# Performance work log

Hardware: AMD Instinct MI355X
Metric: run time of the kernel (lower is better)

Reference implementation:

```python
import jax, jax.numpy as jnp
import numpy as np

A = 200000   # atoms
B = 400000   # directed bonds
H = 300      # hidden_size
AF = 133     # atom_fdim
BF = 147     # bond_fdim
DEPTH = 4    # message passing depth -> DEPTH-1 W_h layers
M = 4096     # molecules in batch


def setup_inputs() -> dict:
    key = jax.random.key(0)
    ks = jax.random.split(key, 10)
    s = 0.05
    f_atoms = jax.random.normal(ks[0], (A, AF), jnp.float32)
    f_bonds = jax.random.normal(ks[1], (B, BF), jnp.float32)
    b_src = jax.random.randint(ks[2], (B,), 0, A, jnp.int32)
    b_dst = jax.random.randint(ks[3], (B,), 0, A, jnp.int32)
    # reverse-bond pairing: bond 2i <-> 2i+1
    b2revb = (jnp.arange(B, dtype=jnp.int32) ^ 1)
    mol_ids = jnp.sort(jax.random.randint(ks[4], (A,), 0, M, jnp.int32))
    W_i_atom = jax.random.normal(ks[5], (AF, H), jnp.float32) * s
    W_i_bond = jax.random.normal(ks[6], (BF, H), jnp.float32) * s
    W_h = jax.random.normal(ks[7], (DEPTH - 1, H, H), jnp.float32) * s
    W_o = jax.random.normal(ks[8], (3 * H, H), jnp.float32) * s
    b_o = jnp.zeros((H,), jnp.float32)
    return dict(f_atoms=f_atoms, f_bonds=f_bonds, W_i_atom=W_i_atom,
                W_i_bond=W_i_bond, W_h=W_h, W_o=W_o, b_o=b_o,
                b_src=b_src, b_dst=b_dst, b2revb=b2revb, mol_ids=mol_ids)


def reference(f_atoms, f_bonds, W_i_atom, W_i_bond, W_h, W_o, b_o,
              b_src, b_dst, b2revb, mol_ids):
    relu = jax.nn.relu
    input_atom = relu(f_atoms @ W_i_atom)   # [A, H]
    input_bond = relu(f_bonds @ W_i_bond)   # [B, H]

    def step(message, Wd):
        # scatter-sum incoming bond messages onto destination atoms
        a_msg = jax.ops.segment_sum(message, b_dst, num_segments=A)  # [A, H]
        # gather back to bonds, subtract reverse-bond message (D-MPNN)
        m = a_msg[b_src] - message[b2revb]                           # [B, H]
        return relu(input_bond + m @ Wd), None

    message, _ = jax.lax.scan(step, input_bond, W_h)  # DEPTH-1 iterations

    a_msg = jax.ops.segment_sum(message, b_dst, num_segments=A)      # [A, H]
    a_input = jnp.concatenate([input_atom, a_msg, input_atom * a_msg], axis=-1)
    atom_h = relu(a_input @ W_o + b_o)                               # [A, H]

    # mean readout per molecule
    sums = jax.ops.segment_sum(atom_h, mol_ids, num_segments=M)      # [M, H]
    counts = jax.ops.segment_sum(jnp.ones((A,), atom_h.dtype), mol_ids, num_segments=M)
    return sums / jnp.clip(counts, 1.0)[:, None]
```

## Files before the change

### kernel.cpp

```cpp
#include <hip/hip_runtime.h>
#include <stdint.h>

#define H   300
#define HP  320
#define CAP 32

using bf8 = __attribute__((ext_vector_type(8))) short;
using s4  = __attribute__((ext_vector_type(4))) short;
using f4  = __attribute__((ext_vector_type(4))) float;

__device__ __forceinline__ float bf2f(unsigned short u){
    union { unsigned int i; float f; } v; v.i = ((unsigned int)u) << 16; return v.f;
}
__device__ __forceinline__ unsigned short f2bf(float x){
    unsigned int u = __builtin_bit_cast(unsigned int, x);
    u = (u + 0x7FFFu + ((u >> 16) & 1u)) >> 16;
    return (unsigned short)u;
}

__global__ void fill_k(const int* __restrict__ b_dst, int* __restrict__ cnt,
                       int* __restrict__ bucket, int nB){
    int e = blockIdx.x * 256 + threadIdx.x;
    if (e >= nB) return;
    int d = b_dst[e];
    int slot = atomicAdd(&cnt[d], 1);
    if (slot < CAP) bucket[(long)d * CAP + slot] = e;
}

__global__ void prep_wt(const float* __restrict__ W, unsigned short* __restrict__ Wt,
                        int Kact, int Kp){
    int idx = blockIdx.x * 256 + threadIdx.x;
    if (idx >= 320 * Kp) return;
    int t  = idx / (320 * 32);
    int r  = idx % (320 * 32);
    int n  = r / 32, kk = r % 32;
    int k  = t * 32 + kk;
    float v = (n < H && k < Kact) ? W[(long)k * H + n] : 0.f;
    Wt[idx] = f2bf(v);
}

__global__ void prep_wto(const float* __restrict__ W, unsigned short* __restrict__ Wt){
    int idx = blockIdx.x * 256 + threadIdx.x;
    if (idx >= 320 * 960) return;
    int t  = idx / (320 * 32);
    int r  = idx % (320 * 32);
    int n  = r / 32, kk = r % 32;
    int k  = t * 32 + kk;
    int sec = k / HP, ksec = k % HP;
    float v = (n < H && ksec < H) ? W[((long)sec * H + ksec) * H + n] : 0.f;
    Wt[idx] = f2bf(v);
}

__global__ __launch_bounds__(256)
void conv_in(const float* __restrict__ X, int rows, int Kact,
             unsigned short* __restrict__ Y){
    int t = blockIdx.x * 256 + threadIdx.x;
    if (t >= rows * 20) return;
    int row = t / 20, c = t % 20;
    int k0 = c * 8;
    bf8 v;
    #pragma unroll
    for (int j = 0; j < 8; j++){
        int k = k0 + j;
        float f = (k < Kact) ? X[(long)row * Kact + k] : 0.f;
        v[j] = (short)f2bf(f);
    }
    *(bf8*)(Y + (long)row * 160 + k0) = v;
}

template<int RL, int SEC, int EPI>
__global__ __launch_bounds__(256, 4)
void gemm_k(const unsigned short* __restrict__ A0,
            const unsigned short* __restrict__ A1,
            const unsigned short* __restrict__ A2,
            const unsigned short* __restrict__ Wt,
            const float* __restrict__ b_o,
            unsigned short* __restrict__ outb,
            int nTiles)
{
    constexpr int KS     = RL / 32;
    constexpr int TS     = SEC * KS;
    constexpr int CHUNKS = RL / 8;
    constexpr int XM     = (RL == 320) ? 7 : 3;
    constexpr int NCH    = 32 * CHUNKS;
    constexpr int ROWB   = RL * 2;

    __shared__ char lds[32 * ROWB];

    const int tid  = threadIdx.x;
    const int w    = tid >> 6;
    const int lane = tid & 63;
    const int lr   = lane & 15;
    const int g    = lane >> 4;

    int tile = blockIdx.x;
    if (tile >= nTiles) return;
    const long rowBase = (long)tile * 32;

    const unsigned short* Ap[3] = {A0, A1, A2};

    auto stageA = [&](int sec){
        const char* gb = (const char*)(Ap[sec] + rowBase * RL);
        bf8 st[(NCH + 255) / 256];
        #pragma unroll
        for (int i = 0; i < (NCH + 255) / 256; i++){
            int f = i * 256 + tid;
            if (NCH % 256 == 0 || f < NCH)
                st[i] = *(const bf8*)(gb + f * 16);
        }
        #pragma unroll
        for (int i = 0; i < (NCH + 255) / 256; i++){
            int f = i * 256 + tid;
            if (NCH % 256 == 0 || f < NCH){
                int row = f / CHUNKS, c = f % CHUNKS;
                *(bf8*)(lds + row * ROWB + ((c ^ (row & XM)) << 4)) = st[i];
            }
        }
    };

    bf8 bb[2][5];
    auto loadB = [&](int t, bf8 (&dst)[5]){
        const unsigned short* base = Wt + ((long)t * 320) * 32 + g * 8;
        #pragma unroll
        for (int n = 0; n < 5; n++)
            dst[n] = *(const bf8*)(base + (w * 80 + n * 16 + lr) * 32);
    };

    f4 acc[2][5];

    #pragma unroll
    for (int sec = 0; sec < SEC; ++sec){
        if (sec > 0) __syncthreads();
        stageA(sec);
        __syncthreads();
        if (sec == 0){
            #pragma unroll
            for (int m = 0; m < 2; m++)
                #pragma unroll
                for (int n = 0; n < 5; n++)
                    acc[m][n] = (f4){0.f, 0.f, 0.f, 0.f};
        }
        loadB(sec * KS + 0, bb[0]);
        if (KS > 1) loadB(sec * KS + 1, bb[1]);

        #pragma unroll
        for (int i = 0; i < KS; i++){
            bf8 af[2];
            #pragma unroll
            for (int m = 0; m < 2; m++){
                int row = m * 16 + lr;
                int ch  = i * 4 + g;
                af[m] = *(const bf8*)(lds + row * ROWB + ((ch ^ (row & XM)) << 4));
            }
            #pragma unroll
            for (int m = 0; m < 2; m++)
                #pragma unroll
                for (int n = 0; n < 5; n++)
                    acc[m][n] = __builtin_amdgcn_mfma_f32_16x16x32_bf16(
                        bb[i & 1][n], af[m], acc[m][n], 0, 0, 0);
            if (i + 2 < KS) loadB(sec * KS + i + 2, bb[i & 1]);
        }
    }

    #pragma unroll
    for (int m = 0; m < 2; m++){
        const long row = rowBase + m * 16 + lr;
        #pragma unroll
        for (int n = 0; n < 5; n++){
            const int colBase = w * 80 + n * 16 + g * 4;
            s4 v4;
            #pragma unroll
            for (int q = 0; q < 4; q++){
                int col = colBase + q;
                float v = acc[m][n][q];
                if constexpr (EPI == 2) v += (col < H ? b_o[col] : 0.f);
                if constexpr (EPI != 1) v = fmaxf(v, 0.f);
                v4[q] = (short)f2bf(v);
            }
            *(s4*)(outb + row * HP + colBase) = v4;
        }
    }
}

__global__ __launch_bounds__(256)
void comb_k(const unsigned short* __restrict__ MW,
            const unsigned short* __restrict__ bond_in,
            const int* __restrict__ b_src, const int* __restrict__ b2revb,
            const int* __restrict__ cnt, const int* __restrict__ bucket,
            unsigned short* __restrict__ out, int nB){
    int t = blockIdx.x * 256 + threadIdx.x;
    if (t >= nB * 40) return;
    int e = t / 40, ch = t % 40;
    int k0 = ch * 8;
    int s   = b_src[e];
    int rev = b2revb[e];
    int dg = cnt[s]; if (dg > CAP) dg = CAP;
    long base = (long)s * CAP;
    int be0 = 0, be1 = 0, be2 = 0, be3 = 0;
    if (dg > 0) be0 = bucket[base + 0];
    if (dg > 1) be1 = bucket[base + 1];
    if (dg > 2) be2 = bucket[base + 2];
    if (dg > 3) be3 = bucket[base + 3];
    bf8 bi = *(const bf8*)(bond_in + (long)e * HP + k0);
    bf8 rv = *(const bf8*)(MW + (long)rev * HP + k0);
    bf8 m0, m1, m2, m3;
    if (dg > 0) m0 = *(const bf8*)(MW + (long)be0 * HP + k0);
    if (dg > 1) m1 = *(const bf8*)(MW + (long)be1 * HP + k0);
    if (dg > 2) m2 = *(const bf8*)(MW + (long)be2 * HP + k0);
    if (dg > 3) m3 = *(const bf8*)(MW + (long)be3 * HP + k0);
    float sacc[8];
    #pragma unroll
    for (int q = 0; q < 8; q++)
        sacc[q] = bf2f((unsigned short)bi[q]) - bf2f((unsigned short)rv[q]);
    auto addv = [&](bf8 mm){
        #pragma unroll
        for (int q = 0; q < 8; q++) sacc[q] += bf2f((unsigned short)mm[q]);
    };
    if (dg > 0) addv(m0);
    if (dg > 1) addv(m1);
    if (dg > 2) addv(m2);
    if (dg > 3) addv(m3);
    for (int j = 4; j < dg; ++j){
        int be = bucket[base + j];
        addv(*(const bf8*)(MW + (long)be * HP + k0));
    }
    bf8 v;
    #pragma unroll
    for (int q = 0; q < 8; q++) v[q] = (short)f2bf(fmaxf(sacc[q], 0.f));
    *(bf8*)(out + (long)e * HP + k0) = v;
}

__global__ __launch_bounds__(256)
void amsg_k(const unsigned short* __restrict__ msg, const int* __restrict__ cnt,
            const int* __restrict__ bucket,
            const unsigned short* __restrict__ input_atom,
            unsigned short* __restrict__ amsg, unsigned short* __restrict__ prod,
            int nA){
    int t = blockIdx.x * 256 + threadIdx.x;
    if (t >= nA * 40) return;
    int a = t / 40, ch = t % 40;
    int k0 = ch * 8;
    int dg = cnt[a]; if (dg > CAP) dg = CAP;
    long base = (long)a * CAP;
    int be0 = 0, be1 = 0, be2 = 0, be3 = 0;
    if (dg > 0) be0 = bucket[base + 0];
    if (dg > 1) be1 = bucket[base + 1];
    if (dg > 2) be2 = bucket[base + 2];
    if (dg > 3) be3 = bucket[base + 3];
    bf8 ia = *(const bf8*)(input_atom + (long)a * HP + k0);
    bf8 m0, m1, m2, m3;
    if (dg > 0) m0 = *(const bf8*)(msg + (long)be0 * HP + k0);
    if (dg > 1) m1 = *(const bf8*)(msg + (long)be1 * HP + k0);
    if (dg > 2) m2 = *(const bf8*)(msg + (long)be2 * HP + k0);
    if (dg > 3) m3 = *(const bf8*)(msg + (long)be3 * HP + k0);
    float s[8];
    #pragma unroll
    for (int q = 0; q < 8; q++) s[q] = 0.f;
    auto addv = [&](bf8 mm){
        #pragma unroll
        for (int q = 0; q < 8; q++) s[q] += bf2f((unsigned short)mm[q]);
    };
    if (dg > 0) addv(m0);
    if (dg > 1) addv(m1);
    if (dg > 2) addv(m2);
    if (dg > 3) addv(m3);
    for (int j = 4; j < dg; ++j)
        addv(*(const bf8*)(msg + (long)bucket[base + j] * HP + k0));
    bf8 va, vp;
    #pragma unroll
    for (int q = 0; q < 8; q++){
        va[q] = (short)f2bf(s[q]);
        vp[q] = (short)f2bf(s[q] * bf2f((unsigned short)ia[q]));
    }
    *(bf8*)(amsg + (long)a * HP + k0) = va;
    *(bf8*)(prod + (long)a * HP + k0) = vp;
}

__global__ __launch_bounds__(320)
void readout_k(const unsigned short* __restrict__ atom_h,
               const int* __restrict__ mol_ids, int nAtoms,
               float* __restrict__ out){
    int m = blockIdx.x;
    int t = threadIdx.x;
    int lo = 0, hi = nAtoms;
    while (lo < hi){ int mid = (lo + hi) >> 1; if (mol_ids[mid] < m) lo = mid + 1; else hi = mid; }
    int lo2 = lo, hi2 = nAtoms;
    while (lo2 < hi2){ int mid = (lo2 + hi2) >> 1; if (mol_ids[mid] < m + 1) lo2 = mid + 1; else hi2 = mid; }
    if (t < H){
        float s = 0.f;
        for (int a = lo; a < lo2; ++a) s += bf2f(atom_h[(long)a * HP + t]);
        int c2 = lo2 - lo;
        out[(long)m * H + t] = s / (float)(c2 > 0 ? c2 : 1);
    }
}

extern "C" void kernel_launch(void* const* d_in, const int* in_sizes, int n_in,
                              void* d_out, int out_size, void* d_ws, size_t ws_size,
                              hipStream_t stream){
    const float* f_atoms  = (const float*)d_in[0];
    const float* f_bonds  = (const float*)d_in[1];
    const float* W_i_atom = (const float*)d_in[2];
    const float* W_i_bond = (const float*)d_in[3];
    const float* W_h      = (const float*)d_in[4];
    const float* W_o      = (const float*)d_in[5];
    const float* b_o      = (const float*)d_in[6];
    const int* b_src   = (const int*)d_in[7];
    const int* b_dst   = (const int*)d_in[8];
    const int* b2revb  = (const int*)d_in[9];
    const int* mol_ids = (const int*)d_in[10];

    const int nA = in_sizes[10];
    const int nB = in_sizes[7];
    const int nM = out_size / H;

    char* p = (char*)d_ws;
    auto alloc = [&](size_t bytes){ char* q = p; p += (bytes + 255) & ~(size_t)255; return q; };
    unsigned short* Wt_ia = (unsigned short*)alloc((size_t)320 * 160 * 2);
    unsigned short* Wt_ib = (unsigned short*)alloc((size_t)320 * 160 * 2);
    unsigned short* Wt_h  = (unsigned short*)alloc((size_t)3 * 320 * 320 * 2);
    unsigned short* Wt_o  = (unsigned short*)alloc((size_t)320 * 960 * 2);
    int* cnt    = (int*)alloc((size_t)nA * 4);
    int* bucket = (int*)alloc((size_t)nA * CAP * 4);
    unsigned short* input_atom = (unsigned short*)alloc((size_t)nA * HP * 2);
    unsigned short* input_bond = (unsigned short*)alloc((size_t)nB * HP * 2);
    unsigned short* msgA = (unsigned short*)alloc((size_t)nB * HP * 2);
    unsigned short* MW   = (unsigned short*)alloc((size_t)nB * HP * 2);
    unsigned short* fa_bf  = MW;
    unsigned short* fb_bf  = MW + (size_t)nA * 160;
    unsigned short* amsg   = MW;
    unsigned short* prod   = MW + (size_t)nA * HP;
    unsigned short* atom_h = input_bond;

    if ((size_t)(p - (char*)d_ws) > ws_size) return;

    hipMemsetAsync(cnt, 0, (size_t)nA * 4, stream);
    fill_k<<<dim3((nB + 255) / 256), dim3(256), 0, stream>>>(b_dst, cnt, bucket, nB);

    prep_wt<<<dim3((320*160 + 255)/256), dim3(256), 0, stream>>>(W_i_atom, Wt_ia, 133, 160);
    prep_wt<<<dim3((320*160 + 255)/256), dim3(256), 0, stream>>>(W_i_bond, Wt_ib, 147, 160);
    for (int d = 0; d < 3; d++)
        prep_wt<<<dim3((320*320 + 255)/256), dim3(256), 0, stream>>>(
            W_h + (size_t)d * H * H, Wt_h + (size_t)d * 320 * 320, 300, 320);
    prep_wto<<<dim3((320*960 + 255)/256), dim3(256), 0, stream>>>(W_o, Wt_o);
    conv_in<<<dim3((nA*20 + 255)/256), dim3(256), 0, stream>>>(f_atoms, nA, 133, fa_bf);
    conv_in<<<dim3((nB*20 + 255)/256), dim3(256), 0, stream>>>(f_bonds, nB, 147, fb_bf);

    const int tilesA = nA / 32, tilesB = nB / 32;

    gemm_k<160,1,0><<<dim3(tilesA), dim3(256), 0, stream>>>(
        fa_bf, nullptr, nullptr, Wt_ia, nullptr, input_atom, tilesA);
    gemm_k<160,1,0><<<dim3(tilesB), dim3(256), 0, stream>>>(
        fb_bf, nullptr, nullptr, Wt_ib, nullptr, input_bond, tilesB);

    const int combGrid = (nB * 40 + 255) / 256;
    const unsigned short* msg_cur = input_bond;
    for (int d = 0; d < 3; d++){
        gemm_k<320,1,1><<<dim3(tilesB), dim3(256), 0, stream>>>(
            msg_cur, nullptr, nullptr, Wt_h + (size_t)d * 320 * 320, nullptr, MW, tilesB);
        comb_k<<<dim3(combGrid), dim3(256), 0, stream>>>(
            MW, input_bond, b_src, b2revb, cnt, bucket, msgA, nB);
        msg_cur = msgA;
    }

    amsg_k<<<dim3((nA * 40 + 255) / 256), dim3(256), 0, stream>>>(
        msgA, cnt, bucket, input_atom, amsg, prod, nA);

    gemm_k<320,3,2><<<dim3(tilesA), dim3(256), 0, stream>>>(
        input_atom, amsg, prod, Wt_o, b_o, atom_h, tilesA);

    readout_k<<<dim3(nM), dim3(320), 0, stream>>>(atom_h, mol_ids, nA, (float*)d_out);
}
```

Measured before the change: 2.208 ms.

## Make GEMM persistent with double-buffered LDS prefetch of next A tile

Converts the GEMM kernel to a grid-stride persistent loop with a fixed grid of 1024 blocks. While the current section computes, the next A tile is loaded into registers and written to a second LDS buffer. The aim is to hide global-load latency behind MFMA work and cut block launch overhead. LDS use doubles, which may lower occupancy, and register pressure rises from the held prefetch registers.

```diff
diff --git a/kernel.cpp b/kernel.cpp
--- a/kernel.cpp
+++ b/kernel.cpp
@@ -79,13 +79,13 @@
             int nTiles)
 {
     constexpr int KS     = RL / 32;
-    constexpr int TS     = SEC * KS;
     constexpr int CHUNKS = RL / 8;
     constexpr int XM     = (RL == 320) ? 7 : 3;
     constexpr int NCH    = 32 * CHUNKS;
     constexpr int ROWB   = RL * 2;
-
-    __shared__ char lds[32 * ROWB];
+    constexpr int NST    = (NCH + 255) / 256;
+
+    __shared__ char lds[2][32 * ROWB];
 
     const int tid  = threadIdx.x;
     const int w    = tid >> 6;
@@ -95,25 +95,27 @@
 
     int tile = blockIdx.x;
     if (tile >= nTiles) return;
-    const long rowBase = (long)tile * 32;
+    const int tstride = gridDim.x;
 
     const unsigned short* Ap[3] = {A0, A1, A2};
 
-    auto stageA = [&](int sec){
-        const char* gb = (const char*)(Ap[sec] + rowBase * RL);
-        bf8 st[(NCH + 255) / 256];
-        #pragma unroll
-        for (int i = 0; i < (NCH + 255) / 256; i++){
+    bf8 st[NST];
+    auto loadA = [&](const unsigned short* src, long rowBase){
+        const char* gb = (const char*)(src + rowBase * RL) + tid * 16;
+        #pragma unroll
+        for (int i = 0; i < NST; i++){
             int f = i * 256 + tid;
             if (NCH % 256 == 0 || f < NCH)
-                st[i] = *(const bf8*)(gb + f * 16);
+                st[i] = *(const bf8*)(gb + i * 4096);
         }
-        #pragma unroll
-        for (int i = 0; i < (NCH + 255) / 256; i++){
+    };
+    auto writeA = [&](int buf){
+        #pragma unroll
+        for (int i = 0; i < NST; i++){
             int f = i * 256 + tid;
             if (NCH % 256 == 0 || f < NCH){
                 int row = f / CHUNKS, c = f % CHUNKS;
-                *(bf8*)(lds + row * ROWB + ((c ^ (row & XM)) << 4)) = st[i];
+                *(bf8*)(lds[buf] + row * ROWB + ((c ^ (row & XM)) << 4)) = st[i];
             }
         }
     };
@@ -128,56 +130,71 @@
 
     f4 acc[2][5];
 
-    #pragma unroll
-    for (int sec = 0; sec < SEC; ++sec){
-        if (sec > 0) __syncthreads();
-        stageA(sec);
-        __syncthreads();
-        if (sec == 0){
+    loadA(Ap[0], (long)tile * 32);
+    writeA(0);
+    __syncthreads();
+    int cur = 0;
+
+    for (; tile < nTiles; tile += tstride){
+        #pragma unroll
+        for (int sec = 0; sec < SEC; ++sec){
+            int ns = sec + 1, ntile = tile;
+            if (ns == SEC){ ns = 0; ntile = tile + tstride; }
+            const bool haveNext = (ntile < nTiles);
+            if (haveNext) loadA(Ap[ns], (long)ntile * 32);
+
+            if (sec == 0){
+                #pragma unroll
+                for (int m = 0; m < 2; m++)
+                    #pragma unroll
+                    for (int n = 0; n < 5; n++)
+                        acc[m][n] = (f4){0.f, 0.f, 0.f, 0.f};
+            }
+            loadB(sec * KS + 0, bb[0]);
+            if (KS > 1) loadB(sec * KS + 1, bb[1]);
+
             #pragma unroll
-            for (int m = 0; m < 2; m++)
+            for (int i = 0; i < KS; i++){
+                bf8 af[2];
                 #pragma unroll
-                for (int n = 0; n < 5; n++)
-                    acc[m][n] = (f4){0.f, 0.f, 0.f, 0.f};
-        }
-        loadB(sec * KS + 0, bb[0]);
-        if (KS > 1) loadB(sec * KS + 1, bb[1]);
-
-        #pragma unroll
-        for (int i = 0; i < KS; i++){
-            bf8 af[2];
-            #pragma unroll
-            for (int m = 0; m < 2; m++){
-                int row = m * 16 + lr;
-                int ch  = i * 4 + g;
-                af[m] = *(const bf8*)(lds + row * ROWB + ((ch ^ (row & XM)) << 4));
+                for (int m = 0; m < 2; m++){
+                    int row = m * 16 + lr;
+                    int ch  = i * 4 + g;
+                    af[m] = *(const bf8*)(lds[cur] + row * ROWB + ((ch ^ (row & XM)) << 4));
+                }
+                #pragma unroll
+                for (int m = 0; m < 2; m++)
+                    #pragma unroll
+                    for (int n = 0; n < 5; n++)
+                        acc[m][n] = __builtin_amdgcn_mfma_f32_16x16x32_bf16(
+                            bb[i & 1][n], af[m], acc[m][n], 0, 0, 0);
+                if (i + 2 < KS) loadB(sec * KS + i + 2, bb[i & 1]);
             }
-            #pragma unroll
-            for (int m = 0; m < 2; m++)
+
+            if (sec == SEC - 1){
                 #pragma unroll
-                for (int n = 0; n < 5; n++)
-                    acc[m][n] = __builtin_amdgcn_mfma_f32_16x16x32_bf16(
-                        bb[i & 1][n], af[m], acc[m][n], 0, 0, 0);
-            if (i + 2 < KS) loadB(sec * KS + i + 2, bb[i & 1]);
-        }
-    }
-
-    #pragma unroll
-    for (int m = 0; m < 2; m++){
-        const long row = rowBase + m * 16 + lr;
-        #pragma unroll
-        for (int n = 0; n < 5; n++){
-            const int colBase = w * 80 + n * 16 + g * 4;
-            s4 v4;
-            #pragma unroll
-            for (int q = 0; q < 4; q++){
-                int col = colBase + q;
-                float v = acc[m][n][q];
-                if constexpr (EPI == 2) v += (col < H ? b_o[col] : 0.f);
-                if constexpr (EPI != 1) v = fmaxf(v, 0.f);
-                v4[q] = (short)f2bf(v);
+                for (int m = 0; m < 2; m++){
+                    const long row = (long)tile * 32 + m * 16 + lr;
+                    #pragma unroll
+                    for (int n = 0; n < 5; n++){
+                        const int colBase = w * 80 + n * 16 + g * 4;
+                        s4 v4;
+                        #pragma unroll
+                        for (int q = 0; q < 4; q++){
+                            int col = colBase + q;
+                            float v = acc[m][n][q];
+                            if constexpr (EPI == 2) v += (col < H ? b_o[col] : 0.f);
+                            if constexpr (EPI != 1) v = fmaxf(v, 0.f);
+                            v4[q] = (short)f2bf(v);
+                        }
+                        *(s4*)(outb + row * HP + colBase) = v4;
+                    }
+                }
             }
-            *(s4*)(outb + row * HP + colBase) = v4;
+
+            if (haveNext) writeA(cur ^ 1);
+            __syncthreads();
+            cur ^= 1;
         }
     }
 }
@@ -346,16 +363,17 @@
     conv_in<<<dim3((nB*20 + 255)/256), dim3(256), 0, stream>>>(f_bonds, nB, 147, fb_bf);
 
     const int tilesA = nA / 32, tilesB = nB / 32;
-
-    gemm_k<160,1,0><<<dim3(tilesA), dim3(256), 0, stream>>>(
+    const int GP = 1024;
+
+    gemm_k<160,1,0><<<dim3(GP), dim3(256), 0, stream>>>(
         fa_bf, nullptr, nullptr, Wt_ia, nullptr, input_atom, tilesA);
-    gemm_k<160,1,0><<<dim3(tilesB), dim3(256), 0, stream>>>(
+    gemm_k<160,1,0><<<dim3(GP), dim3(256), 0, stream>>>(
         fb_bf, nullptr, nullptr, Wt_ib, nullptr, input_bond, tilesB);
 
     const int combGrid = (nB * 40 + 255) / 256;
     const unsigned short* msg_cur = input_bond;
     for (int d = 0; d < 3; d++){
-        gemm_k<320,1,1><<<dim3(tilesB), dim3(256), 0, stream>>>(
+        gemm_k<320,1,1><<<dim3(GP), dim3(256), 0, stream>>>(
             msg_cur, nullptr, nullptr, Wt_h + (size_t)d * 320 * 320, nullptr, MW, tilesB);
         comb_k<<<dim3(combGrid), dim3(256), 0, stream>>>(
             MW, input_bond, b_src, b2revb, cnt, bucket, msgA, nB);
@@ -365,7 +383,7 @@
     amsg_k<<<dim3((nA * 40 + 255) / 256), dim3(256), 0, stream>>>(
         msgA, cnt, bucket, input_atom, amsg, prod, nA);
 
-    gemm_k<320,3,2><<<dim3(tilesA), dim3(256), 0, stream>>>(
+    gemm_k<320,3,2><<<dim3(GP), dim3(256), 0, stream>>>(
         input_atom, amsg, prod, Wt_o, b_o, atom_h, tilesA);
 
     readout_k<<<dim3(nM), dim3(320), 0, stream>>>(atom_h, mol_ids, nA, (float*)d_out);
```

New measurement: 4.485 ms. +103.1%, slower.

## Use tiled chunk-major activation layout with persistent B-stationary GEMM and LDS DMA

Applied to the files above, without the earlier changes.

Switches all bf16 activation buffers from row-major to a tiled chunk-major layout, where 32 or 64 rows of each 8-element column chunk are stored contiguously. The input and W_h GEMMs become a persistent kernel of 256 blocks. Each block keeps half of the weight matrix resident in LDS, splits N between block pairs, and double-buffers A tiles with global_load_lds DMA. The aim is to stop reloading weights per tile and to make A staging a straight copy without swizzling, at the cost of one block per CU, large LDS use, and more scattered addressing in the gather kernels.

```diff
diff --git a/kernel.cpp b/kernel.cpp
--- a/kernel.cpp
+++ b/kernel.cpp
@@ -16,6 +16,13 @@
     unsigned int u = __builtin_bit_cast(unsigned int, x);
     u = (u + 0x7FFFu + ((u >> 16) & 1u)) >> 16;
     return (unsigned short)u;
+}
+
+__device__ __forceinline__ long a320(long row, int ch){
+    return (row >> 5) * 10240 + (long)ch * 256 + (row & 31) * 8;
+}
+__device__ __forceinline__ long a160(long row, int ch){
+    return (row >> 6) * 10240 + (long)ch * 512 + (row & 63) * 8;
 }
 
 __global__ void fill_k(const int* __restrict__ b_dst, int* __restrict__ cnt,
@@ -65,27 +72,119 @@
         float f = (k < Kact) ? X[(long)row * Kact + k] : 0.f;
         v[j] = (short)f2bf(f);
     }
-    *(bf8*)(Y + (long)row * 160 + k0) = v;
-}
-
-template<int RL, int SEC, int EPI>
+    *(bf8*)(Y + a160(row, c)) = v;
+}
+
+template<int RL, int BM, int EPI>
+__global__ __launch_bounds__(256, 1)
+void bstat_k(const unsigned short* __restrict__ A,
+             const unsigned short* __restrict__ Wt,
+             unsigned short* __restrict__ outb,
+             int nTiles)
+{
+    constexpr int T     = RL / 32;
+    constexpr int MF    = BM / 32;
+    constexpr int TILEB = BM * RL * 2;
+
+    __shared__ char ldsB[T * 10240];
+    __shared__ char ldsA[2][TILEB];
+
+    const int tid  = threadIdx.x;
+    const int w    = tid >> 6;
+    const int wm   = w >> 1, wn = w & 1;
+    const int lane = tid & 63;
+    const int lr   = lane & 15;
+    const int g    = lane >> 4;
+    const int nh   = blockIdx.x & 1;
+
+    for (int idx = tid; idx < T * 640; idx += 256){
+        int t  = idx / 640;
+        int r  = idx - t * 640;
+        int gg = r / 160;
+        int n  = r - gg * 160;
+        bf8 v = *(const bf8*)(Wt + ((long)t * 320 + nh * 160 + n) * 32 + gg * 8);
+        *(bf8*)(ldsB + (long)idx * 16) = v;
+    }
+
+    auto dma = [&](int t, int buf){
+        const char* g0 = (const char*)A + (long)t * TILEB + tid * 16;
+        char* l0 = ldsA[buf] + (w * 64) * 16;
+        #pragma unroll
+        for (int rd = 0; rd < 5; rd++)
+            __builtin_amdgcn_global_load_lds(
+                (const __attribute__((address_space(1))) void*)(g0 + rd * 4096),
+                (__attribute__((address_space(3))) void*)(l0 + rd * 4096),
+                16, 0, 0);
+    };
+
+    int tile = blockIdx.x >> 1;
+    if (tile < nTiles) dma(tile, 0);
+    __syncthreads();
+
+    int buf = 0;
+    for (; tile < nTiles; tile += 128){
+        int nt = tile + 128;
+        if (nt < nTiles) dma(nt, buf ^ 1);
+
+        f4 acc[MF][5];
+        #pragma unroll
+        for (int mf = 0; mf < MF; mf++)
+            #pragma unroll
+            for (int nf = 0; nf < 5; nf++)
+                acc[mf][nf] = (f4){0.f, 0.f, 0.f, 0.f};
+
+        #pragma unroll
+        for (int t = 0; t < T; t++){
+            bf8 bfr[5], af[MF];
+            const char* bb = ldsB + (((t * 4 + g) * 160) + wn * 80 + lr) * 16;
+            #pragma unroll
+            for (int nf = 0; nf < 5; nf++)
+                bfr[nf] = *(const bf8*)(bb + nf * 256);
+            #pragma unroll
+            for (int mf = 0; mf < MF; mf++)
+                af[mf] = *(const bf8*)(ldsA[buf] +
+                    ((t * 4 + g) * BM + wm * (BM / 2) + mf * 16 + lr) * 16);
+            #pragma unroll
+            for (int mf = 0; mf < MF; mf++)
+                #pragma unroll
+                for (int nf = 0; nf < 5; nf++)
+                    acc[mf][nf] = __builtin_amdgcn_mfma_f32_16x16x32_bf16(
+                        bfr[nf], af[mf], acc[mf][nf], 0, 0, 0);
+        }
+
+        #pragma unroll
+        for (int mf = 0; mf < MF; mf++){
+            const long row = (long)tile * BM + wm * (BM / 2) + mf * 16 + lr;
+            #pragma unroll
+            for (int nf = 0; nf < 5; nf++){
+                const int colg = nh * 160 + wn * 80 + nf * 16 + g * 4;
+                s4 v4;
+                #pragma unroll
+                for (int q = 0; q < 4; q++){
+                    float v = acc[mf][nf][q];
+                    if constexpr (EPI == 0) v = fmaxf(v, 0.f);
+                    v4[q] = (short)f2bf(v);
+                }
+                *(s4*)(outb + a320(row, colg >> 3) + (colg & 7)) = v4;
+            }
+        }
+        __syncthreads();
+        buf ^= 1;
+    }
+}
+
 __global__ __launch_bounds__(256, 4)
-void gemm_k(const unsigned short* __restrict__ A0,
-            const unsigned short* __restrict__ A1,
-            const unsigned short* __restrict__ A2,
-            const unsigned short* __restrict__ Wt,
-            const float* __restrict__ b_o,
-            unsigned short* __restrict__ outb,
-            int nTiles)
+void gemm_wo(const unsigned short* __restrict__ A0,
+             const unsigned short* __restrict__ A1,
+             const unsigned short* __restrict__ A2,
+             const unsigned short* __restrict__ Wt,
+             const float* __restrict__ b_o,
+             unsigned short* __restrict__ outb,
+             int nTiles)
 {
-    constexpr int KS     = RL / 32;
-    constexpr int TS     = SEC * KS;
-    constexpr int CHUNKS = RL / 8;
-    constexpr int XM     = (RL == 320) ? 7 : 3;
-    constexpr int NCH    = 32 * CHUNKS;
-    constexpr int ROWB   = RL * 2;
-
-    __shared__ char lds[32 * ROWB];
+    constexpr int KS = 10;
+
+    __shared__ char lds[20480];
 
     const int tid  = threadIdx.x;
     const int w    = tid >> 6;
@@ -95,27 +194,18 @@
 
     int tile = blockIdx.x;
     if (tile >= nTiles) return;
-    const long rowBase = (long)tile * 32;
 
     const unsigned short* Ap[3] = {A0, A1, A2};
 
     auto stageA = [&](int sec){
-        const char* gb = (const char*)(Ap[sec] + rowBase * RL);
-        bf8 st[(NCH + 255) / 256];
-        #pragma unroll
-        for (int i = 0; i < (NCH + 255) / 256; i++){
-            int f = i * 256 + tid;
-            if (NCH % 256 == 0 || f < NCH)
-                st[i] = *(const bf8*)(gb + f * 16);
-        }
-        #pragma unroll
-        for (int i = 0; i < (NCH + 255) / 256; i++){
-            int f = i * 256 + tid;
-            if (NCH % 256 == 0 || f < NCH){
-                int row = f / CHUNKS, c = f % CHUNKS;
-                *(bf8*)(lds + row * ROWB + ((c ^ (row & XM)) << 4)) = st[i];
-            }
-        }
+        const char* gb = (const char*)(Ap[sec] + (long)tile * 10240);
+        bf8 st[5];
+        #pragma unroll
+        for (int i = 0; i < 5; i++)
+            st[i] = *(const bf8*)(gb + (i * 256 + tid) * 16);
+        #pragma unroll
+        for (int i = 0; i < 5; i++)
+            *(bf8*)(lds + (i * 256 + tid) * 16) = st[i];
     };
 
     bf8 bb[2][5];
@@ -127,31 +217,26 @@
     };
 
     f4 acc[2][5];
-
-    #pragma unroll
-    for (int sec = 0; sec < SEC; ++sec){
+    #pragma unroll
+    for (int m = 0; m < 2; m++)
+        #pragma unroll
+        for (int n = 0; n < 5; n++)
+            acc[m][n] = (f4){0.f, 0.f, 0.f, 0.f};
+
+    #pragma unroll
+    for (int sec = 0; sec < 3; ++sec){
         if (sec > 0) __syncthreads();
         stageA(sec);
+        loadB(sec * KS + 0, bb[0]);
         __syncthreads();
-        if (sec == 0){
-            #pragma unroll
-            for (int m = 0; m < 2; m++)
-                #pragma unroll
-                for (int n = 0; n < 5; n++)
-                    acc[m][n] = (f4){0.f, 0.f, 0.f, 0.f};
-        }
-        loadB(sec * KS + 0, bb[0]);
-        if (KS > 1) loadB(sec * KS + 1, bb[1]);
+        loadB(sec * KS + 1, bb[1]);
 
         #pragma unroll
         for (int i = 0; i < KS; i++){
             bf8 af[2];
             #pragma unroll
-            for (int m = 0; m < 2; m++){
-                int row = m * 16 + lr;
-                int ch  = i * 4 + g;
-                af[m] = *(const bf8*)(lds + row * ROWB + ((ch ^ (row & XM)) << 4));
-            }
+            for (int m = 0; m < 2; m++)
+                af[m] = *(const bf8*)(lds + ((i * 4 + g) * 32 + m * 16 + lr) * 16);
             #pragma unroll
             for (int m = 0; m < 2; m++)
                 #pragma unroll
@@ -164,20 +249,19 @@
 
     #pragma unroll
     for (int m = 0; m < 2; m++){
-        const long row = rowBase + m * 16 + lr;
+        const long row = (long)tile * 32 + m * 16 + lr;
         #pragma unroll
         for (int n = 0; n < 5; n++){
-            const int colBase = w * 80 + n * 16 + g * 4;
+            const int colg = w * 80 + n * 16 + g * 4;
             s4 v4;
             #pragma unroll
             for (int q = 0; q < 4; q++){
-                int col = colBase + q;
+                int col = colg + q;
                 float v = acc[m][n][q];
-                if constexpr (EPI == 2) v += (col < H ? b_o[col] : 0.f);
-                if constexpr (EPI != 1) v = fmaxf(v, 0.f);
-                v4[q] = (short)f2bf(v);
+                v += (col < H ? b_o[col] : 0.f);
+                v4[q] = (short)f2bf(fmaxf(v, 0.f));
             }
-            *(s4*)(outb + row * HP + colBase) = v4;
+            *(s4*)(outb + a320(row, colg >> 3) + (colg & 7)) = v4;
         }
     }
 }
@@ -191,7 +275,6 @@
     int t = blockIdx.x * 256 + threadIdx.x;
     if (t >= nB * 40) return;
     int e = t / 40, ch = t % 40;
-    int k0 = ch * 8;
     int s   = b_src[e];
     int rev = b2revb[e];
     int dg = cnt[s]; if (dg > CAP) dg = CAP;
@@ -201,13 +284,13 @@
     if (dg > 1) be1 = bucket[base + 1];
     if (dg > 2) be2 = bucket[base + 2];
     if (dg > 3) be3 = bucket[base + 3];
-    bf8 bi = *(const bf8*)(bond_in + (long)e * HP + k0);
-    bf8 rv = *(const bf8*)(MW + (long)rev * HP + k0);
+    bf8 bi = *(const bf8*)(bond_in + a320(e, ch));
+    bf8 rv = *(const bf8*)(MW + a320(rev, ch));
     bf8 m0, m1, m2, m3;
-    if (dg > 0) m0 = *(const bf8*)(MW + (long)be0 * HP + k0);
-    if (dg > 1) m1 = *(const bf8*)(MW + (long)be1 * HP + k0);
-    if (dg > 2) m2 = *(const bf8*)(MW + (long)be2 * HP + k0);
-    if (dg > 3) m3 = *(const bf8*)(MW + (long)be3 * HP + k0);
+    if (dg > 0) m0 = *(const bf8*)(MW + a320(be0, ch));
+    if (dg > 1) m1 = *(const bf8*)(MW + a320(be1, ch));
+    if (dg > 2) m2 = *(const bf8*)(MW + a320(be2, ch));
+    if (dg > 3) m3 = *(const bf8*)(MW + a320(be3, ch));
     float sacc[8];
     #pragma unroll
     for (int q = 0; q < 8; q++)
@@ -222,12 +305,12 @@
     if (dg > 3) addv(m3);
     for (int j = 4; j < dg; ++j){
         int be = bucket[base + j];
-        addv(*(const bf8*)(MW + (long)be * HP + k0));
+        addv(*(const bf8*)(MW + a320(be, ch)));
     }
     bf8 v;
     #pragma unroll
     for (int q = 0; q < 8; q++) v[q] = (short)f2bf(fmaxf(sacc[q], 0.f));
-    *(bf8*)(out + (long)e * HP + k0) = v;
+    *(bf8*)(out + a320(e, ch)) = v;
 }
 
 __global__ __launch_bounds__(256)
@@ -239,7 +322,6 @@
     int t = blockIdx.x * 256 + threadIdx.x;
     if (t >= nA * 40) return;
     int a = t / 40, ch = t % 40;
-    int k0 = ch * 8;
     int dg = cnt[a]; if (dg > CAP) dg = CAP;
     long base = (long)a * CAP;
     int be0 = 0, be1 = 0, be2 = 0, be3 = 0;
@@ -247,12 +329,12 @@
     if (dg > 1) be1 = bucket[base + 1];
     if (dg > 2) be2 = bucket[base + 2];
     if (dg > 3) be3 = bucket[base + 3];
-    bf8 ia = *(const bf8*)(input_atom + (long)a * HP + k0);
+    bf8 ia = *(const bf8*)(input_atom + a320(a, ch));
     bf8 m0, m1, m2, m3;
-    if (dg > 0) m0 = *(const bf8*)(msg + (long)be0 * HP + k0);
-    if (dg > 1) m1 = *(const bf8*)(msg + (long)be1 * HP + k0);
-    if (dg > 2) m2 = *(const bf8*)(msg + (long)be2 * HP + k0);
-    if (dg > 3) m3 = *(const bf8*)(msg + (long)be3 * HP + k0);
+    if (dg > 0) m0 = *(const bf8*)(msg + a320(be0, ch));
+    if (dg > 1) m1 = *(const bf8*)(msg + a320(be1, ch));
+    if (dg > 2) m2 = *(const bf8*)(msg + a320(be2, ch));
+    if (dg > 3) m3 = *(const bf8*)(msg + a320(be3, ch));
     float s[8];
     #pragma unroll
     for (int q = 0; q < 8; q++) s[q] = 0.f;
@@ -265,15 +347,15 @@
     if (dg > 2) addv(m2);
     if (dg > 3) addv(m3);
     for (int j = 4; j < dg; ++j)
-        addv(*(const bf8*)(msg + (long)bucket[base + j] * HP + k0));
+        addv(*(const bf8*)(msg + a320(bucket[base + j], ch)));
     bf8 va, vp;
     #pragma unroll
     for (int q = 0; q < 8; q++){
         va[q] = (short)f2bf(s[q]);
         vp[q] = (short)f2bf(s[q] * bf2f((unsigned short)ia[q]));
     }
-    *(bf8*)(amsg + (long)a * HP + k0) = va;
-    *(bf8*)(prod + (long)a * HP + k0) = vp;
+    *(bf8*)(amsg + a320(a, ch)) = va;
+    *(bf8*)(prod + a320(a, ch)) = vp;
 }
 
 __global__ __launch_bounds__(320)
@@ -287,8 +369,10 @@
     int lo2 = lo, hi2 = nAtoms;
     while (lo2 < hi2){ int mid = (lo2 + hi2) >> 1; if (mol_ids[mid] < m + 1) lo2 = mid + 1; else hi2 = mid; }
     if (t < H){
+        int ch = t >> 3, j = t & 7;
         float s = 0.f;
-        for (int a = lo; a < lo2; ++a) s += bf2f(atom_h[(long)a * HP + t]);
+        for (int a = lo; a < lo2; ++a)
+            s += bf2f(atom_h[a320(a, ch) + j]);
         int c2 = lo2 - lo;
         out[(long)m * H + t] = s / (float)(c2 > 0 ? c2 : 1);
     }
@@ -345,18 +429,16 @@
     conv_in<<<dim3((nA*20 + 255)/256), dim3(256), 0, stream>>>(f_atoms, nA, 133, fa_bf);
     conv_in<<<dim3((nB*20 + 255)/256), dim3(256), 0, stream>>>(f_bonds, nB, 147, fb_bf);
 
-    const int tilesA = nA / 32, tilesB = nB / 32;
-
-    gemm_k<160,1,0><<<dim3(tilesA), dim3(256), 0, stream>>>(
-        fa_bf, nullptr, nullptr, Wt_ia, nullptr, input_atom, tilesA);
-    gemm_k<160,1,0><<<dim3(tilesB), dim3(256), 0, stream>>>(
-        fb_bf, nullptr, nullptr, Wt_ib, nullptr, input_bond, tilesB);
+    bstat_k<160,64,0><<<dim3(256), dim3(256), 0, stream>>>(
+        fa_bf, Wt_ia, input_atom, nA / 64);
+    bstat_k<160,64,0><<<dim3(256), dim3(256), 0, stream>>>(
+        fb_bf, Wt_ib, input_bond, nB / 64);
 
     const int combGrid = (nB * 40 + 255) / 256;
     const unsigned short* msg_cur = input_bond;
     for (int d = 0; d < 3; d++){
-        gemm_k<320,1,1><<<dim3(tilesB), dim3(256), 0, stream>>>(
-            msg_cur, nullptr, nullptr, Wt_h + (size_t)d * 320 * 320, nullptr, MW, tilesB);
+        bstat_k<320,32,1><<<dim3(256), dim3(256), 0, stream>>>(
+            msg_cur, Wt_h + (size_t)d * 320 * 320, MW, nB / 32);
         comb_k<<<dim3(combGrid), dim3(256), 0, stream>>>(
             MW, input_bond, b_src, b2revb, cnt, bucket, msgA, nB);
         msg_cur = msgA;
@@ -365,8 +447,8 @@
     amsg_k<<<dim3((nA * 40 + 255) / 256), dim3(256), 0, stream>>>(
         msgA, cnt, bucket, input_atom, amsg, prod, nA);
 
-    gemm_k<320,3,2><<<dim3(tilesA), dim3(256), 0, stream>>>(
-        input_atom, amsg, prod, Wt_o, b_o, atom_h, tilesA);
+    gemm_wo<<<dim3(nA / 32), dim3(256), 0, stream>>>(
+        input_atom, amsg, prod, Wt_o, b_o, atom_h, nA / 32);
 
     readout_k<<<dim3(nM), dim3(320), 0, stream>>>(atom_h, mol_ids, nA, (float*)d_out);
 }
```

After: 4.355 ms. 1.97x slower.
